# Optimization experiments

Measured on AMD Instinct MI355X. Metric: run time of the kernel, lower is better.

## Reference

```python
import jax, jax.numpy as jnp
import numpy as np

# Poincare ball with curvature c = 1 (geoopt defaults)
_BOUND = 1.0 - 1e-5  # keep points strictly inside the unit ball for arctanh


def _norm(x):
    return jnp.maximum(jnp.sqrt(jnp.sum(x * x, axis=-1, keepdims=True)), 1e-15)


def expmap0(u):
    n = _norm(u)
    return jnp.tanh(n) * u / n


def logmap0(x):
    n = _norm(x)
    return jnp.arctanh(jnp.minimum(n, _BOUND)) * x / n


def mobius_add(x, y):
    x2 = jnp.sum(x * x, axis=-1, keepdims=True)
    y2 = jnp.sum(y * y, axis=-1, keepdims=True)
    xy = jnp.sum(x * y, axis=-1, keepdims=True)
    num = (1.0 + 2.0 * xy + y2) * x + (1.0 - x2) * y
    den = 1.0 + 2.0 * xy + x2 * y2
    return num / jnp.maximum(den, 1e-15)


def poincare_linear(x, W, b=None):
    # logmap0 -> euclidean linear (no bias) -> expmap0 -> mobius bias add
    y = expmap0(logmap0(x) @ W)
    if b is not None:
        y = mobius_add(y, b)
    return y


def setup_inputs() -> dict:
    key = jax.random.key(0)
    ks = jax.random.split(key, 11)
    N, IN1, IN2, H, OUT = 524288, 32, 32, 64, 32

    def on_ball(k, n, d, scale=0.3):
        return expmap0(scale * jax.random.normal(k, (n, d), dtype=jnp.float32))

    x1 = on_ball(ks[0], N, IN1)
    x2 = on_ball(ks[1], N, IN2)
    # weights stored as [in, out] (transpose of torch nn.Linear layout)
    Wc1 = jax.random.normal(ks[2], (IN1, H), dtype=jnp.float32) / np.sqrt(IN1)
    Wc2 = jax.random.normal(ks[3], (IN2, H), dtype=jnp.float32) / np.sqrt(IN2)
    bc = on_ball(ks[4], 1, H, scale=0.1)
    W0 = jax.random.normal(ks[5], (H, H), dtype=jnp.float32) / np.sqrt(H)
    b0 = on_ball(ks[6], 1, H, scale=0.1)
    W1 = jax.random.normal(ks[7], (H, OUT), dtype=jnp.float32) / np.sqrt(H)
    b1 = on_ball(ks[8], 1, OUT, scale=0.1)
    return {"x1": x1, "x2": x2, "Wc1": Wc1, "Wc2": Wc2, "bc": bc,
            "W0": W0, "b0": b0, "W1": W1, "b1": b1}


def reference(x1, x2, Wc1, Wc2, bc, W0, b0, W1, b1):
    # PoincareConcat: two bias-free PoincareLinear branches, mobius-added, then bias
    h1 = poincare_linear(x1, Wc1)
    h2 = poincare_linear(x2, Wc2)
    h = mobius_add(mobius_add(h1, h2), bc)
    # SingleInputPoincareMLP: PoincareLinear(64->64), PoincareLinear(64->32)
    h = poincare_linear(h, W0, b0)
    h = poincare_linear(h, W1, b1)
    return h
```

## Files before the change

### kernel.cpp

```cpp
#include <hip/hip_runtime.h>
#include <math.h>


typedef short bf16x8 __attribute__((ext_vector_type(8)));
typedef float f32x4  __attribute__((ext_vector_type(4)));

#define MFMA16(A, B, C) __builtin_amdgcn_mfma_f32_16x16x32_bf16((A), (B), (C), 0, 0, 0)
#define PBOUND 0.99999f

static __device__ __forceinline__ float artanh_c(float n) {
    float z = fminf(n, PBOUND);
    return 0.5f * __logf((1.0f + z) / (1.0f - z));
}
static __device__ __forceinline__ float tanh_pos(float n) {
    float e = __expf(-2.0f * n);
    return (1.0f - e) / (1.0f + e);
}
static __device__ __forceinline__ float red4q(float v) {
    v += __shfl_xor(v, 16);
    v += __shfl_xor(v, 32);
    return v;
}
static __device__ __forceinline__ void split_trunc(float x, short* h, short* l) {
    unsigned u = __builtin_bit_cast(unsigned, x);
    *h = (short)(u >> 16);
    float fh = __builtin_bit_cast(float, u & 0xFFFF0000u);
    float r = x - fh;
    unsigned ur = __builtin_bit_cast(unsigned, r);
    *l = (short)(ur >> 16);
}

static __device__ __forceinline__ int kperm(int kk) {
    return 32 * (kk >> 5) + 16 * ((kk & 7) >> 2) + 4 * ((kk >> 3) & 3) + (kk & 3);
}

template <int NT>
static __device__ __forceinline__ float dotred(const f32x4* a, const f32x4* b) {
    float p = 0.0f;
#pragma unroll
    for (int t = 0; t < NT; ++t)
#pragma unroll
        for (int r = 0; r < 4; ++r) p = fmaf(a[t][r], b[t][r], p);
    return red4q(p);
}

template <int NT>
static __device__ __forceinline__ void expmap_fold(const f32x4* d, float& lam, float& X2) {
    float p = 0.0f;
#pragma unroll
    for (int t = 0; t < NT; ++t)
#pragma unroll
        for (int r = 0; r < 4; ++r) p = fmaf(d[t][r], d[t][r], p);
    p = red4q(p);
    float nU = fmaxf(lam * sqrtf(p), 1e-15f);
    float th = tanh_pos(nU);
    lam = lam * th / nU;
    X2 = th * th;
}

static __device__ __forceinline__ void logmap_fold(float& lam, float X2) {
    float n = fmaxf(sqrtf(X2), 1e-15f);
    lam *= artanh_c(n) / n;
}

template <int NT>
static __device__ __forceinline__ void mobius_bias_fold(f32x4* d, const f32x4* bv,
                                                        float& lam, float& X2, float b2) {
    float C = dotred<NT>(d, bv);
    float xy = lam * C;
    float a = 1.0f + 2.0f * xy + b2;
    float b = 1.0f - X2;
    float den = fmaxf(fmaf(X2, b2, 1.0f + 2.0f * xy), 1e-15f);
    float inv = 1.0f / den;
    float A = a * lam;
#pragma unroll
    for (int t = 0; t < NT; ++t)
#pragma unroll
        for (int r = 0; r < 4; ++r) d[t][r] = fmaf(A, d[t][r], b * bv[t][r]);
    lam = inv;
    X2 = (a * a * X2 + 2.0f * a * b * xy + b * b * b2) * (inv * inv);
}

static __device__ __forceinline__ void split_d16(const f32x4* d, bf16x8* bh, bf16x8* bl) {
#pragma unroll
    for (int kt = 0; kt < 2; ++kt)
#pragma unroll
        for (int jj = 0; jj < 8; ++jj) {
            short hh, ll;
            split_trunc(d[2 * kt + (jj >> 2)][jj & 3], &hh, &ll);
            bh[kt][jj] = hh;
            bl[kt][jj] = ll;
        }
}

template <int NT>
static __device__ __forceinline__ void layer_mm(const bf16x8* F, int fbase,
                                                int lane, const bf16x8* ah,
                                                const bf16x8* al, f32x4* d) {
#pragma unroll
    for (int t = 0; t < NT; ++t) {
        f32x4 c = {0.0f, 0.0f, 0.0f, 0.0f};
#pragma unroll
        for (int kt = 0; kt < 2; ++kt) {
            int f = fbase + 2 * t + kt;
            bf16x8 wh = F[(2 * f) * 64 + lane];
            bf16x8 wl = F[(2 * f + 1) * 64 + lane];
            c = MFMA16(wh, ah[kt], c);
            c = MFMA16(wl, ah[kt], c);
            c = MFMA16(wh, al[kt], c);
        }
        d[t] = c;
    }
}

static __device__ __forceinline__ void branch_stage(const float* __restrict__ x, size_t row,
                                                    int q, int lane, int fbase,
                                                    const bf16x8* F, f32x4* d,
                                                    float& lam, float& X2) {
    const float4* p4 = (const float4*)(x + row * 32 + q * 8);
    float4 va = p4[0], vb = p4[1];
    float v[8] = {va.x, va.y, va.z, va.w, vb.x, vb.y, vb.z, vb.w};
    float n2 = 0.0f;
#pragma unroll
    for (int i = 0; i < 8; ++i) n2 = fmaf(v[i], v[i], n2);
    n2 = red4q(n2);
    float n = fmaxf(sqrtf(n2), 1e-15f);
    lam = artanh_c(n) / n;
    bf16x8 bh, bl;
#pragma unroll
    for (int i = 0; i < 8; ++i) {
        short hh, ll;
        split_trunc(v[i], &hh, &ll);
        bh[i] = hh;
        bl[i] = ll;
    }
#pragma unroll
    for (int t = 0; t < 4; ++t) {
        bf16x8 wh = F[(2 * (fbase + t)) * 64 + lane];
        bf16x8 wl = F[(2 * (fbase + t) + 1) * 64 + lane];
        f32x4 c = {0.0f, 0.0f, 0.0f, 0.0f};
        c = MFMA16(wh, bh, c);
        c = MFMA16(wl, bh, c);
        c = MFMA16(wh, bl, c);
        d[t] = c;
    }
    expmap_fold<4>(d, lam, X2);
}

__global__ void build_frags(const float* __restrict__ Wc1, const float* __restrict__ Wc2,
                            const float* __restrict__ W0, const float* __restrict__ W1,
                            const float* __restrict__ bc, const float* __restrict__ b0,
                            const float* __restrict__ b1, unsigned short* __restrict__ fout,
                            float* __restrict__ norms) {
    int tid = blockIdx.x * blockDim.x + threadIdx.x;
    const int total = 40 * 512;
    if (tid < total) {
        int p = tid >> 9, within = tid & 511;
        int lane = within >> 3, jj = within & 7;
        int f = p >> 1, isLo = p & 1;
        int m = lane & 15, kq = lane >> 4;
        int kl = kq * 8 + jj;
        float w;
        if (f < 4)      w = Wc1[kl * 64 + f * 16 + m];
        else if (f < 8) w = Wc2[kl * 64 + (f - 4) * 16 + m];
        else if (f < 16) {
            int t = (f - 8) >> 1, kt = (f - 8) & 1;
            w = W0[kperm(32 * kt + kl) * 64 + t * 16 + m];
        } else {
            int t = (f - 16) >> 1, kt = (f - 16) & 1;
            w = W1[kperm(32 * kt + kl) * 32 + t * 16 + m];
        }
        unsigned u = __builtin_bit_cast(unsigned, w);
        unsigned r = u + (0x7FFFu + ((u >> 16) & 1u));
        unsigned short hi = (unsigned short)(r >> 16);
        float fhi = __builtin_bit_cast(float, (unsigned)hi << 16);
        float res = w - fhi;
        unsigned ul = __builtin_bit_cast(unsigned, res);
        unsigned rl = ul + (0x7FFFu + ((ul >> 16) & 1u));
        fout[tid] = isLo ? (unsigned short)(rl >> 16) : hi;
    } else if (tid < total + 3) {
        int which = tid - total;
        const float* b = which == 0 ? bc : (which == 1 ? b0 : b1);
        int n = which == 2 ? 32 : 64;
        float s = 0.0f;
        for (int i = 0; i < n; ++i) s += b[i] * b[i];
        norms[which] = s;
    }
}

__global__ void __launch_bounds__(256, 4) poincare_mfma4(
    const float* __restrict__ x1, const float* __restrict__ x2,
    const float* __restrict__ bc, const float* __restrict__ b0,
    const float* __restrict__ b1, const unsigned short* __restrict__ frags,
    const float* __restrict__ norms, float* __restrict__ out, int ntiles) {
    __shared__ __align__(16) unsigned short smem[20480];

    const int tid = threadIdx.x;
    {
        const uint4* g = (const uint4*)frags;
        uint4* s = (uint4*)smem;
#pragma unroll
        for (int i = 0; i < 10; ++i) s[tid + i * 256] = g[tid + i * 256];
    }
    __syncthreads();

    const int lane = tid & 63;
    const int wid = tid >> 6;
    const int tile = blockIdx.x * 4 + wid;
    if (tile >= ntiles) return;
    const int j = lane & 15, q = lane >> 4;
    const size_t row = (size_t)tile * 16 + j;

    const bf16x8* F = (const bf16x8*)smem;
    const float bc2 = norms[0], b02 = norms[1], b12 = norms[2];

    f32x4 d1[4], d2[4];
    float lam1, X2, lam2, Y2;
    branch_stage(x1, row, q, lane, 0, F, d1, lam1, X2);
    branch_stage(x2, row, q, lane, 4, F, d2, lam2, Y2);

    {
        float C = dotred<4>(d1, d2);
        float xy = lam1 * lam2 * C;
        float a = 1.0f + 2.0f * xy + Y2;
        float b = 1.0f - X2;
        float den = fmaxf(fmaf(X2, Y2, 1.0f + 2.0f * xy), 1e-15f);
        float inv = 1.0f / den;
        float A = a * lam1, B = b * lam2;
#pragma unroll
        for (int t = 0; t < 4; ++t)
#pragma unroll
            for (int r = 0; r < 4; ++r) d1[t][r] = fmaf(A, d1[t][r], B * d2[t][r]);
        lam1 = inv;
        X2 = (a * a * X2 + 2.0f * a * b * xy + b * b * Y2) * (inv * inv);
    }
    f32x4 bcv[4];
#pragma unroll
    for (int t = 0; t < 4; ++t) bcv[t] = *(const f32x4*)(bc + t * 16 + q * 4);
    mobius_bias_fold<4>(d1, bcv, lam1, X2, bc2);
    logmap_fold(lam1, X2);

    bf16x8 ah[2], al[2];
    split_d16(d1, ah, al);
    f32x4 d0[4];
    layer_mm<4>(F, 8, lane, ah, al, d0);
    expmap_fold<4>(d0, lam1, X2);
    f32x4 b0v[4];
#pragma unroll
    for (int t = 0; t < 4; ++t) b0v[t] = *(const f32x4*)(b0 + t * 16 + q * 4);
    mobius_bias_fold<4>(d0, b0v, lam1, X2, b02);
    logmap_fold(lam1, X2);

    split_d16(d0, ah, al);
    f32x4 dO[2];
    layer_mm<2>(F, 16, lane, ah, al, dO);
    expmap_fold<2>(dO, lam1, X2);

    f32x4 b1v[2];
#pragma unroll
    for (int t = 0; t < 2; ++t) b1v[t] = *(const f32x4*)(b1 + t * 16 + q * 4);
    {
        float C = dotred<2>(dO, b1v);
        float xy = lam1 * C;
        float a = 1.0f + 2.0f * xy + b12;
        float b = 1.0f - X2;
        float den = fmaxf(fmaf(X2, b12, 1.0f + 2.0f * xy), 1e-15f);
        float inv = 1.0f / den;
        float F1 = inv * a * lam1, F2 = inv * b;
#pragma unroll
        for (int t = 0; t < 2; ++t) {
            f32x4 res;
#pragma unroll
            for (int r = 0; r < 4; ++r) res[r] = fmaf(F1, dO[t][r], F2 * b1v[t][r]);
            *(f32x4*)(out + row * 32 + t * 16 + q * 4) = res;
        }
    }
}

extern "C" void kernel_launch(void* const* d_in, const int* in_sizes, int n_in,
                              void* d_out, int out_size, void* d_ws, size_t ws_size,
                              hipStream_t stream) {
    const float* x1  = (const float*)d_in[0];
    const float* x2  = (const float*)d_in[1];
    const float* Wc1 = (const float*)d_in[2];
    const float* Wc2 = (const float*)d_in[3];
    const float* bc  = (const float*)d_in[4];
    const float* W0  = (const float*)d_in[5];
    const float* b0  = (const float*)d_in[6];
    const float* W1  = (const float*)d_in[7];
    const float* b1  = (const float*)d_in[8];
    float* out = (float*)d_out;

    unsigned short* frags = (unsigned short*)d_ws;
    float* norms = (float*)((char*)d_ws + 40 * 512 * 2);

    const int nrows  = in_sizes[0] / 32;
    const int ntiles = nrows / 16;
    const int nblocks = (ntiles + 3) / 4;

    build_frags<<<81, 256, 0, stream>>>(Wc1, Wc2, W0, W1, bc, b0, b1, frags, norms);
    poincare_mfma4<<<nblocks, 256, 0, stream>>>(x1, x2, bc, b0, b1, frags, norms, out, ntiles);
}
```

Baseline: 202.9 us.

## Switch to 32x32x16 bf16 MFMA with 32-row tiles per wavefront

Replaces the 16x16x32 MFMA tiling with 32x32x16 MFMA, so each wavefront handles 32 rows instead of 16. The weight fragment layout and k-permutation are rebuilt to match the new operand layout, and cross-lane reductions drop from two shuffles to one. The aim is to halve the number of tiles and cut per-row shuffle and overhead cost. In exchange the wider accumulators raise register pressure, and the row loads become less contiguous per lane.

```diff
diff --git a/kernel.cpp b/kernel.cpp
--- a/kernel.cpp
+++ b/kernel.cpp
@@ -4,8 +4,9 @@
 
 typedef short bf16x8 __attribute__((ext_vector_type(8)));
 typedef float f32x4  __attribute__((ext_vector_type(4)));
-
-#define MFMA16(A, B, C) __builtin_amdgcn_mfma_f32_16x16x32_bf16((A), (B), (C), 0, 0, 0)
+typedef float f32x16 __attribute__((ext_vector_type(16)));
+
+#define MFMA32(A, B, C) __builtin_amdgcn_mfma_f32_32x32x16_bf16((A), (B), (C), 0, 0, 0)
 #define PBOUND 0.99999f
 
 static __device__ __forceinline__ float artanh_c(float n) {
@@ -16,10 +17,8 @@
     float e = __expf(-2.0f * n);
     return (1.0f - e) / (1.0f + e);
 }
-static __device__ __forceinline__ float red4q(float v) {
-    v += __shfl_xor(v, 16);
-    v += __shfl_xor(v, 32);
-    return v;
+static __device__ __forceinline__ float red2h(float v) {
+    return v + __shfl_xor(v, 32);
 }
 static __device__ __forceinline__ void split_trunc(float x, short* h, short* l) {
     unsigned u = __builtin_bit_cast(unsigned, x);
@@ -30,28 +29,36 @@
     *l = (short)(ur >> 16);
 }
 
-static __device__ __forceinline__ int kperm(int kk) {
-    return 32 * (kk >> 5) + 16 * ((kk & 7) >> 2) + 4 * ((kk >> 3) & 3) + (kk & 3);
-}
-
-template <int NT>
-static __device__ __forceinline__ float dotred(const f32x4* a, const f32x4* b) {
+static __device__ __forceinline__ int kperm32(int s) {
+    return (s >> 5) * 32 + (((s >> 2) & 1) + 2 * ((s >> 4) & 1)) * 8 +
+           ((s >> 3) & 1) * 4 + (s & 3);
+}
+
+static __device__ __forceinline__ f32x16 zero16() {
+    f32x16 z;
+#pragma unroll
+    for (int r = 0; r < 16; ++r) z[r] = 0.0f;
+    return z;
+}
+
+template <int NV>
+static __device__ __forceinline__ float dotred32(const f32x16* a, const f32x16* b) {
     float p = 0.0f;
 #pragma unroll
-    for (int t = 0; t < NT; ++t)
-#pragma unroll
-        for (int r = 0; r < 4; ++r) p = fmaf(a[t][r], b[t][r], p);
-    return red4q(p);
-}
-
-template <int NT>
-static __device__ __forceinline__ void expmap_fold(const f32x4* d, float& lam, float& X2) {
+    for (int v = 0; v < NV; ++v)
+#pragma unroll
+        for (int r = 0; r < 16; ++r) p = fmaf(a[v][r], b[v][r], p);
+    return red2h(p);
+}
+
+template <int NV>
+static __device__ __forceinline__ void expmap_fold32(const f32x16* d, float& lam, float& X2) {
     float p = 0.0f;
 #pragma unroll
-    for (int t = 0; t < NT; ++t)
-#pragma unroll
-        for (int r = 0; r < 4; ++r) p = fmaf(d[t][r], d[t][r], p);
-    p = red4q(p);
+    for (int v = 0; v < NV; ++v)
+#pragma unroll
+        for (int r = 0; r < 16; ++r) p = fmaf(d[v][r], d[v][r], p);
+    p = red2h(p);
     float nU = fmaxf(lam * sqrtf(p), 1e-15f);
     float th = tanh_pos(nU);
     lam = lam * th / nU;
@@ -63,10 +70,10 @@
     lam *= artanh_c(n) / n;
 }
 
-template <int NT>
-static __device__ __forceinline__ void mobius_bias_fold(f32x4* d, const f32x4* bv,
-                                                        float& lam, float& X2, float b2) {
-    float C = dotred<NT>(d, bv);
+template <int NV>
+static __device__ __forceinline__ void mobius_bias_fold32(f32x16* d, const f32x16* bv,
+                                                          float& lam, float& X2, float b2) {
+    float C = dotred32<NV>(d, bv);
     float xy = lam * C;
     float a = 1.0f + 2.0f * xy + b2;
     float b = 1.0f - X2;
@@ -74,77 +81,98 @@
     float inv = 1.0f / den;
     float A = a * lam;
 #pragma unroll
-    for (int t = 0; t < NT; ++t)
-#pragma unroll
-        for (int r = 0; r < 4; ++r) d[t][r] = fmaf(A, d[t][r], b * bv[t][r]);
+    for (int v = 0; v < NV; ++v)
+#pragma unroll
+        for (int r = 0; r < 16; ++r) d[v][r] = fmaf(A, d[v][r], b * bv[v][r]);
     lam = inv;
     X2 = (a * a * X2 + 2.0f * a * b * xy + b * b * b2) * (inv * inv);
 }
 
-static __device__ __forceinline__ void split_d16(const f32x4* d, bf16x8* bh, bf16x8* bl) {
-#pragma unroll
-    for (int kt = 0; kt < 2; ++kt)
-#pragma unroll
-        for (int jj = 0; jj < 8; ++jj) {
+static __device__ __forceinline__ void split_d32(const f32x16 d[2], bf16x8 bh[4], bf16x8 bl[4]) {
+#pragma unroll
+    for (int kt = 0; kt < 4; ++kt)
+#pragma unroll
+        for (int j = 0; j < 8; ++j) {
             short hh, ll;
-            split_trunc(d[2 * kt + (jj >> 2)][jj & 3], &hh, &ll);
-            bh[kt][jj] = hh;
-            bl[kt][jj] = ll;
-        }
+            split_trunc(d[kt >> 1][8 * (kt & 1) + j], &hh, &ll);
+            bh[kt][j] = hh;
+            bl[kt][j] = ll;
+        }
+}
+
+static __device__ __forceinline__ f32x16 loadb(const float* __restrict__ b, int off, int h) {
+    f32x16 r;
+#pragma unroll
+    for (int g = 0; g < 4; ++g) {
+        f32x4 v = *(const f32x4*)(b + off + g * 8 + h * 4);
+#pragma unroll
+        for (int k = 0; k < 4; ++k) r[g * 4 + k] = v[k];
+    }
+    return r;
 }
 
 template <int NT>
-static __device__ __forceinline__ void layer_mm(const bf16x8* F, int fbase,
-                                                int lane, const bf16x8* ah,
-                                                const bf16x8* al, f32x4* d) {
+static __device__ __forceinline__ void layer_mm32(const bf16x8* F, int fbase, int lane,
+                                                  const bf16x8 ah[4], const bf16x8 al[4],
+                                                  f32x16* d) {
 #pragma unroll
     for (int t = 0; t < NT; ++t) {
-        f32x4 c = {0.0f, 0.0f, 0.0f, 0.0f};
-#pragma unroll
-        for (int kt = 0; kt < 2; ++kt) {
-            int f = fbase + 2 * t + kt;
+        f32x16 c = zero16();
+#pragma unroll
+        for (int kt = 0; kt < 4; ++kt) {
+            int f = fbase + t * 4 + kt;
             bf16x8 wh = F[(2 * f) * 64 + lane];
             bf16x8 wl = F[(2 * f + 1) * 64 + lane];
-            c = MFMA16(wh, ah[kt], c);
-            c = MFMA16(wl, ah[kt], c);
-            c = MFMA16(wh, al[kt], c);
+            c = MFMA32(wh, ah[kt], c);
+            c = MFMA32(wl, ah[kt], c);
+            c = MFMA32(wh, al[kt], c);
         }
         d[t] = c;
     }
 }
 
-static __device__ __forceinline__ void branch_stage(const float* __restrict__ x, size_t row,
-                                                    int q, int lane, int fbase,
-                                                    const bf16x8* F, f32x4* d,
-                                                    float& lam, float& X2) {
-    const float4* p4 = (const float4*)(x + row * 32 + q * 8);
-    float4 va = p4[0], vb = p4[1];
-    float v[8] = {va.x, va.y, va.z, va.w, vb.x, vb.y, vb.z, vb.w};
+static __device__ __forceinline__ void branch_stage32(const float* __restrict__ x, size_t row,
+                                                      int h, int lane, int fbase,
+                                                      const bf16x8* F, f32x16* d,
+                                                      float& lam, float& X2) {
+    const float* base = x + row * 32 + h * 8;
+    f32x4 va = *(const f32x4*)(base);
+    f32x4 vb = *(const f32x4*)(base + 4);
+    f32x4 vc = *(const f32x4*)(base + 16);
+    f32x4 vd = *(const f32x4*)(base + 20);
+    float v[16] = {va[0], va[1], va[2], va[3], vb[0], vb[1], vb[2], vb[3],
+                   vc[0], vc[1], vc[2], vc[3], vd[0], vd[1], vd[2], vd[3]};
     float n2 = 0.0f;
 #pragma unroll
-    for (int i = 0; i < 8; ++i) n2 = fmaf(v[i], v[i], n2);
-    n2 = red4q(n2);
+    for (int i = 0; i < 16; ++i) n2 = fmaf(v[i], v[i], n2);
+    n2 = red2h(n2);
     float n = fmaxf(sqrtf(n2), 1e-15f);
     lam = artanh_c(n) / n;
-    bf16x8 bh, bl;
-#pragma unroll
-    for (int i = 0; i < 8; ++i) {
-        short hh, ll;
-        split_trunc(v[i], &hh, &ll);
-        bh[i] = hh;
-        bl[i] = ll;
-    }
-#pragma unroll
-    for (int t = 0; t < 4; ++t) {
-        bf16x8 wh = F[(2 * (fbase + t)) * 64 + lane];
-        bf16x8 wl = F[(2 * (fbase + t) + 1) * 64 + lane];
-        f32x4 c = {0.0f, 0.0f, 0.0f, 0.0f};
-        c = MFMA16(wh, bh, c);
-        c = MFMA16(wl, bh, c);
-        c = MFMA16(wh, bl, c);
+    bf16x8 bh[2], bl[2];
+#pragma unroll
+    for (int kt = 0; kt < 2; ++kt)
+#pragma unroll
+        for (int j = 0; j < 8; ++j) {
+            short hh, ll;
+            split_trunc(v[kt * 8 + j], &hh, &ll);
+            bh[kt][j] = hh;
+            bl[kt][j] = ll;
+        }
+#pragma unroll
+    for (int t = 0; t < 2; ++t) {
+        f32x16 c = zero16();
+#pragma unroll
+        for (int kt = 0; kt < 2; ++kt) {
+            int f = fbase + t * 2 + kt;
+            bf16x8 wh = F[(2 * f) * 64 + lane];
+            bf16x8 wl = F[(2 * f + 1) * 64 + lane];
+            c = MFMA32(wh, bh[kt], c);
+            c = MFMA32(wl, bh[kt], c);
+            c = MFMA32(wh, bl[kt], c);
+        }
         d[t] = c;
     }
-    expmap_fold<4>(d, lam, X2);
+    expmap_fold32<2>(d, lam, X2);
 }
 
 __global__ void build_frags(const float* __restrict__ Wc1, const float* __restrict__ Wc2,
@@ -158,17 +186,21 @@
         int p = tid >> 9, within = tid & 511;
         int lane = within >> 3, jj = within & 7;
         int f = p >> 1, isLo = p & 1;
-        int m = lane & 15, kq = lane >> 4;
-        int kl = kq * 8 + jj;
+        int m = lane & 31, ha = lane >> 5;
+        int kin = ha * 8 + jj;
         float w;
-        if (f < 4)      w = Wc1[kl * 64 + f * 16 + m];
-        else if (f < 8) w = Wc2[kl * 64 + (f - 4) * 16 + m];
-        else if (f < 16) {
-            int t = (f - 8) >> 1, kt = (f - 8) & 1;
-            w = W0[kperm(32 * kt + kl) * 64 + t * 16 + m];
+        if (f < 4) {
+            int t = f >> 1, kt = f & 1;
+            w = Wc1[(kt * 16 + kin) * 64 + t * 32 + m];
+        } else if (f < 8) {
+            int g = f - 4, t = g >> 1, kt = g & 1;
+            w = Wc2[(kt * 16 + kin) * 64 + t * 32 + m];
+        } else if (f < 16) {
+            int g = f - 8, t = g >> 2, kt = g & 3;
+            w = W0[kperm32(kt * 16 + kin) * 64 + t * 32 + m];
         } else {
-            int t = (f - 16) >> 1, kt = (f - 16) & 1;
-            w = W1[kperm(32 * kt + kl) * 32 + t * 16 + m];
+            int kt = f - 16;
+            w = W1[kperm32(kt * 16 + kin) * 32 + m];
         }
         unsigned u = __builtin_bit_cast(unsigned, w);
         unsigned r = u + (0x7FFFu + ((u >> 16) & 1u));
@@ -188,7 +220,7 @@
     }
 }
 
-__global__ void __launch_bounds__(256, 4) poincare_mfma4(
+__global__ void __launch_bounds__(256, 4) poincare_mfma6(
     const float* __restrict__ x1, const float* __restrict__ x2,
     const float* __restrict__ bc, const float* __restrict__ b0,
     const float* __restrict__ b1, const unsigned short* __restrict__ frags,
@@ -208,19 +240,19 @@
     const int wid = tid >> 6;
     const int tile = blockIdx.x * 4 + wid;
     if (tile >= ntiles) return;
-    const int j = lane & 15, q = lane >> 4;
-    const size_t row = (size_t)tile * 16 + j;
+    const int r = lane & 31, h = lane >> 5;
+    const size_t row = (size_t)tile * 32 + r;
 
     const bf16x8* F = (const bf16x8*)smem;
     const float bc2 = norms[0], b02 = norms[1], b12 = norms[2];
 
-    f32x4 d1[4], d2[4];
+    f32x16 d1[2], d2[2];
     float lam1, X2, lam2, Y2;
-    branch_stage(x1, row, q, lane, 0, F, d1, lam1, X2);
-    branch_stage(x2, row, q, lane, 4, F, d2, lam2, Y2);
+    branch_stage32(x1, row, h, lane, 0, F, d1, lam1, X2);
+    branch_stage32(x2, row, h, lane, 4, F, d2, lam2, Y2);
 
     {
-        float C = dotred<4>(d1, d2);
+        float C = dotred32<2>(d1, d2);
         float xy = lam1 * lam2 * C;
         float a = 1.0f + 2.0f * xy + Y2;
         float b = 1.0f - X2;
@@ -228,39 +260,37 @@
         float inv = 1.0f / den;
         float A = a * lam1, B = b * lam2;
 #pragma unroll
-        for (int t = 0; t < 4; ++t)
-#pragma unroll
-            for (int r = 0; r < 4; ++r) d1[t][r] = fmaf(A, d1[t][r], B * d2[t][r]);
+        for (int t = 0; t < 2; ++t)
+#pragma unroll
+            for (int rr = 0; rr < 16; ++rr) d1[t][rr] = fmaf(A, d1[t][rr], B * d2[t][rr]);
         lam1 = inv;
         X2 = (a * a * X2 + 2.0f * a * b * xy + b * b * Y2) * (inv * inv);
     }
-    f32x4 bcv[4];
-#pragma unroll
-    for (int t = 0; t < 4; ++t) bcv[t] = *(const f32x4*)(bc + t * 16 + q * 4);
-    mobius_bias_fold<4>(d1, bcv, lam1, X2, bc2);
+    f32x16 bcv[2];
+#pragma unroll
+    for (int t = 0; t < 2; ++t) bcv[t] = loadb(bc, t * 32, h);
+    mobius_bias_fold32<2>(d1, bcv, lam1, X2, bc2);
     logmap_fold(lam1, X2);
 
-    bf16x8 ah[2], al[2];
-    split_d16(d1, ah, al);
-    f32x4 d0[4];
-    layer_mm<4>(F, 8, lane, ah, al, d0);
-    expmap_fold<4>(d0, lam1, X2);
-    f32x4 b0v[4];
-#pragma unroll
-    for (int t = 0; t < 4; ++t) b0v[t] = *(const f32x4*)(b0 + t * 16 + q * 4);
-    mobius_bias_fold<4>(d0, b0v, lam1, X2, b02);
+    bf16x8 ah[4], al[4];
+    split_d32(d1, ah, al);
+    f32x16 d0[2];
+    layer_mm32<2>(F, 8, lane, ah, al, d0);
+    expmap_fold32<2>(d0, lam1, X2);
+    f32x16 b0v[2];
+#pragma unroll
+    for (int t = 0; t < 2; ++t) b0v[t] = loadb(b0, t * 32, h);
+    mobius_bias_fold32<2>(d0, b0v, lam1, X2, b02);
     logmap_fold(lam1, X2);
 
-    split_d16(d0, ah, al);
-    f32x4 dO[2];
-    layer_mm<2>(F, 16, lane, ah, al, dO);
-    expmap_fold<2>(dO, lam1, X2);
-
-    f32x4 b1v[2];
-#pragma unroll
-    for (int t = 0; t < 2; ++t) b1v[t] = *(const f32x4*)(b1 + t * 16 + q * 4);
+    split_d32(d0, ah, al);
+    f32x16 dO[1];
+    layer_mm32<1>(F, 16, lane, ah, al, dO);
+    expmap_fold32<1>(dO, lam1, X2);
+
+    f32x16 b1v = loadb(b1, 0, h);
     {
-        float C = dotred<2>(dO, b1v);
+        float C = dotred32<1>(dO, &b1v);
         float xy = lam1 * C;
         float a = 1.0f + 2.0f * xy + b12;
         float b = 1.0f - X2;
@@ -268,11 +298,12 @@
         float inv = 1.0f / den;
         float F1 = inv * a * lam1, F2 = inv * b;
 #pragma unroll
-        for (int t = 0; t < 2; ++t) {
+        for (int g = 0; g < 4; ++g) {
             f32x4 res;
 #pragma unroll
-            for (int r = 0; r < 4; ++r) res[r] = fmaf(F1, dO[t][r], F2 * b1v[t][r]);
-            *(f32x4*)(out + row * 32 + t * 16 + q * 4) = res;
+            for (int k = 0; k < 4; ++k)
+                res[k] = fmaf(F1, dO[0][g * 4 + k], F2 * b1v[g * 4 + k]);
+            *(f32x4*)(out + row * 32 + g * 8 + h * 4) = res;
         }
     }
 }
@@ -295,9 +326,9 @@
     float* norms = (float*)((char*)d_ws + 40 * 512 * 2);
 
     const int nrows  = in_sizes[0] / 32;
-    const int ntiles = nrows / 16;
+    const int ntiles = nrows / 32;
     const int nblocks = (ntiles + 3) / 4;
 
     build_frags<<<81, 256, 0, stream>>>(Wc1, Wc2, W0, W1, bc, b0, b1, frags, norms);
-    poincare_mfma4<<<nblocks, 256, 0, stream>>>(x1, x2, bc, b0, b1, frags, norms, out, ntiles);
-}
+    poincare_mfma6<<<nblocks, 256, 0, stream>>>(x1, x2, bc, b0, b1, frags, norms, out, ntiles);
+}
```

Result: no change. 199.5 us (-1.7%).
